# Optimization experiments

Measured on AMD Instinct MI355X. Metric: run time of the kernel, lower is better.

Reference implementation:

```python
import jax, jax.numpy as jnp
import numpy as np

CAPACITY_FACTOR = 1.25


def setup_inputs() -> dict:
    key = jax.random.key(0)
    k1, k2, k3, k4 = jax.random.split(key, 4)
    B, T, H = 2, 2048, 1024
    E, F = 8, 2048
    x = jax.random.normal(k1, (B, T, H), dtype=jnp.float32)
    Wr = jax.random.normal(k2, (H, E), dtype=jnp.float32) * 0.02
    W1 = jax.random.normal(k3, (E, H, 2 * F), dtype=jnp.float32) * 0.02
    W2 = jax.random.normal(k4, (E, F, H), dtype=jnp.float32) * 0.02
    return {"x": x, "Wr": Wr, "W1": W1, "W2": W2}


def _moe_forward(x, Wr, W1, W2):
    B, T, H = x.shape
    E = Wr.shape[1]
    N = B * T
    cap = max(1, int(CAPACITY_FACTOR * (N * 2 / E)))  # static (shape-derived)

    flat_x = x.reshape(N, H)
    logits = flat_x @ Wr                      # [N, E] (train=False: no noise)
    gate = jax.nn.softmax(logits, axis=-1)
    top2_val, top2_idx = jax.lax.top_k(gate, 2)   # [N,2]

    # --- capacity bookkeeping, matching the torch sequential fill order ---
    e0, e1 = top2_idx[:, 0], top2_idx[:, 1]
    oh0 = jax.nn.one_hot(e0, E, dtype=jnp.int32)  # [N,E]
    oh1 = jax.nn.one_hot(e1, E, dtype=jnp.int32)
    # rank of each token within its expert's k=0 queue (flattened token order)
    pos0 = jnp.take_along_axis(jnp.cumsum(oh0, axis=0), top2_idx[:, :1], axis=1)[:, 0] - 1
    count0 = oh0.sum(axis=0)                      # tokens routed top-1 per expert
    used0 = jnp.minimum(count0, cap)              # slots consumed in k=0 pass
    keep0 = pos0 < cap
    # k=1 pass starts after the slots used by k=0
    pos1 = jnp.take_along_axis(jnp.cumsum(oh1, axis=0), top2_idx[:, 1:2], axis=1)[:, 0] - 1
    pos1 = pos1 + used0[e1]
    keep1 = pos1 < cap

    dummy = E * cap  # drop slot
    slot0 = jnp.where(keep0, e0 * cap + pos0, dummy)
    slot1 = jnp.where(keep1, e1 * cap + pos1, dummy)

    # --- dispatch: [E*cap+1, H] buffer (last row is the drop slot) ---
    buf = jnp.zeros((E * cap + 1, H), dtype=x.dtype)
    buf = buf.at[slot0].set(flat_x).at[slot1].set(flat_x)
    xe = buf[: E * cap].reshape(E, cap, H)

    # --- grouped expert FFN (SwiGLU) ---
    h = jnp.einsum("ech,ehf->ecf", xe, W1)        # [E, cap, 2F]
    a, b = jnp.split(h, 2, axis=-1)
    act = jax.nn.silu(a) * b                      # [E, cap, F]
    out = jnp.einsum("ecf,efh->ech", act, W2)     # [E, cap, H]
    out_flat = out.reshape(E * cap, H)

    # --- combine: gather back per token, weighted by gate values ---
    g0 = out_flat[jnp.where(keep0, slot0, 0)] * keep0[:, None]
    g1 = out_flat[jnp.where(keep1, slot1, 0)] * keep1[:, None]
    y = g0 * top2_val[:, 0:1] + g1 * top2_val[:, 1:2]
    y = y.reshape(B, T, H)

    # --- balance loss ---
    me = 1e-9
    prob_per_expert = gate.mean(axis=0)                 # == mean over (B,T)
    used1 = (oh1 * keep1[:, None].astype(jnp.int32)).sum(axis=0)
    used = (used0 + used1).astype(gate.dtype)
    frac_used = jnp.maximum(used, me) / (N * 2 + me)
    balance_loss = (prob_per_expert * frac_used).sum() * E
    return y, balance_loss


def reference(x, Wr, W1, W2):
    return _moe_forward(x, Wr, W1, W2)
```

## Files before the change

### kernel.cpp

```cpp
#include <hip/hip_runtime.h>
#include <cstdint>

#define E_    8
#define H_    1024
#define F_    2048
#define NTOK  4096
#define CAP   1280
#define ECAP  (E_*CAP)

typedef unsigned short u16;
typedef __attribute__((ext_vector_type(8))) short bf16x8;
typedef __attribute__((ext_vector_type(4))) float f32x4;
typedef __attribute__((ext_vector_type(4))) unsigned short u16x4;

__device__ __forceinline__ u16 f2bf(float f) {
  union { float f; uint32_t u; } v; v.f = f;
  uint32_t r = v.u + 0x7fffu + ((v.u >> 16) & 1u);
  return (u16)(r >> 16);
}

__device__ __forceinline__ void gld16(const void* gsrc, void* ldst) {
  auto g = reinterpret_cast<const __attribute__((address_space(1))) uint32_t*>(
      reinterpret_cast<uintptr_t>(gsrc));
  auto l = reinterpret_cast<__attribute__((address_space(3))) uint32_t*>(
      reinterpret_cast<uintptr_t>(ldst));
  __builtin_amdgcn_global_load_lds(g, l, 16, 0, 0);
}

__device__ __forceinline__ int swz(int row, int chunk) {
  return row * 64 + ((chunk ^ (row & 7)) * 8);
}

__global__ __launch_bounds__(256) void prep_kernel(const float* __restrict__ W1,
                                                   const float* __restrict__ W2,
                                                   u16* __restrict__ W1T,
                                                   u16* __restrict__ W2T,
                                                   const float* __restrict__ x,
                                                   const float* __restrict__ Wr,
                                                   int* __restrict__ e0o, int* __restrict__ e1o,
                                                   float* __restrict__ v0o, float* __restrict__ v1o,
                                                   float* __restrict__ partial) {
  int b = blockIdx.x;
  if (b < 12288) {
    __shared__ float tile[64][65];
    const float* in; u16* outp; int R, C, rt, ct;
    if (b < 8192) {
      int slab = b >> 10, t = b & 1023;
      rt = t >> 6; ct = t & 63;
      R = H_; C = 2 * F_;
      in = W1 + (size_t)slab * R * C;
      outp = W1T + (size_t)slab * R * C;
    } else {
      int bb = b - 8192;
      int slab = bb >> 9, t = bb & 511;
      rt = t >> 4; ct = t & 15;
      R = F_; C = H_;
      in = W2 + (size_t)slab * R * C;
      outp = W2T + (size_t)slab * R * C;
    }
    int r0 = rt * 64, c0 = ct * 64;
    int tx = threadIdx.x & 15, ty = threadIdx.x >> 4;
#pragma unroll
    for (int i = 0; i < 4; i++) {
      int row = ty + 16 * i;
      float4 v = *(const float4*)(in + (size_t)(r0 + row) * C + c0 + tx * 4);
      tile[row][tx * 4 + 0] = v.x;
      tile[row][tx * 4 + 1] = v.y;
      tile[row][tx * 4 + 2] = v.z;
      tile[row][tx * 4 + 3] = v.w;
    }
    __syncthreads();
#pragma unroll
    for (int i = 0; i < 4; i++) {
      int c = ty + 16 * i;
      u16x4 bq;
      bq.x = f2bf(tile[tx * 4 + 0][c]);
      bq.y = f2bf(tile[tx * 4 + 1][c]);
      bq.z = f2bf(tile[tx * 4 + 2][c]);
      bq.w = f2bf(tile[tx * 4 + 3][c]);
      *(u16x4*)(outp + (size_t)(c0 + c) * R + r0 + tx * 4) = bq;
    }
  } else {
    int blk = b - 12288;
    int w = threadIdx.x >> 6, l = threadIdx.x & 63;
    int t = blk * 4 + w;
    const float* xr = x + (size_t)t * H_;
    float acc[8] = {0.f,0.f,0.f,0.f,0.f,0.f,0.f,0.f};
#pragma unroll
    for (int it = 0; it < 16; ++it) {
      int h = it * 64 + l;
      float xv = xr[h];
      const float4* wr = (const float4*)(Wr + h * 8);
      float4 wa = wr[0], wb = wr[1];
      acc[0] += xv * wa.x; acc[1] += xv * wa.y; acc[2] += xv * wa.z; acc[3] += xv * wa.w;
      acc[4] += xv * wb.x; acc[5] += xv * wb.y; acc[6] += xv * wb.z; acc[7] += xv * wb.w;
    }
#pragma unroll
    for (int e = 0; e < 8; ++e)
#pragma unroll
      for (int off = 32; off; off >>= 1)
        acc[e] += __shfl_xor(acc[e], off);

    __shared__ float pg[4][8];
    if (l == 0) {
      float mx = acc[0];
#pragma unroll
      for (int e = 1; e < 8; ++e) mx = fmaxf(mx, acc[e]);
      float g[8], s = 0.f;
#pragma unroll
      for (int e = 0; e < 8; ++e) { g[e] = __expf(acc[e] - mx); s += g[e]; }
      float inv = 1.f / s;
#pragma unroll
      for (int e = 0; e < 8; ++e) g[e] *= inv;
      int b0 = 0; float m0 = g[0];
#pragma unroll
      for (int e = 1; e < 8; ++e) if (g[e] > m0) { m0 = g[e]; b0 = e; }
      int b1 = -1; float m1 = -1.f;
#pragma unroll
      for (int e = 0; e < 8; ++e) if (e != b0 && g[e] > m1) { m1 = g[e]; b1 = e; }
      e0o[t] = b0; e1o[t] = b1; v0o[t] = m0; v1o[t] = m1;
#pragma unroll
      for (int e = 0; e < 8; ++e) pg[w][e] = g[e];
    }
    __syncthreads();
    if (threadIdx.x < 8) {
      int e = threadIdx.x;
      partial[blk * 8 + e] = pg[0][e] + pg[1][e] + pg[2][e] + pg[3][e];
    }
  }
}

__global__ __launch_bounds__(256) void scan_kernel(const int* __restrict__ e0i, const int* __restrict__ e1i,
                                                   const float* __restrict__ partial,
                                                   int* __restrict__ slot0, int* __restrict__ slot1,
                                                   int* __restrict__ used_out,
                                                   float* __restrict__ bl_out) {
  __shared__ int c0[256][8], c1[256][8];
  __shared__ float gs[256][8];
  __shared__ int used0_s[8], tot1_s[8];
  int tid = threadIdx.x;

  int le0[16], le1[16];
  int lc0[8] = {0,0,0,0,0,0,0,0}, lc1[8] = {0,0,0,0,0,0,0,0};
  for (int i = 0; i < 16; ++i) {
    int t = tid * 16 + i;
    le0[i] = e0i[t]; le1[i] = e1i[t];
    lc0[le0[i]]++; lc1[le1[i]]++;
  }
#pragma unroll
  for (int e = 0; e < 8; ++e) { c0[tid][e] = lc0[e]; c1[tid][e] = lc1[e]; }

  float g[8] = {0.f,0.f,0.f,0.f,0.f,0.f,0.f,0.f};
  for (int rr = 0; rr < 4; ++rr)
#pragma unroll
    for (int e = 0; e < 8; ++e) g[e] += partial[(tid + rr * 256) * 8 + e];
#pragma unroll
  for (int e = 0; e < 8; ++e) gs[tid][e] = g[e];
  __syncthreads();

  for (int d = 1; d < 256; d <<= 1) {
    int t0[8], t1[8];
    bool a = (tid >= d);
    if (a) {
#pragma unroll
      for (int e = 0; e < 8; ++e) { t0[e] = c0[tid - d][e]; t1[e] = c1[tid - d][e]; }
    }
    __syncthreads();
    if (a) {
#pragma unroll
      for (int e = 0; e < 8; ++e) { c0[tid][e] += t0[e]; c1[tid][e] += t1[e]; }
    }
    __syncthreads();
  }
  for (int s = 128; s > 0; s >>= 1) {
    if (tid < s)
#pragma unroll
      for (int e = 0; e < 8; ++e) gs[tid][e] += gs[tid + s][e];
    __syncthreads();
  }
  if (tid < 8) {
    int e = tid;
    int u0 = min(c0[255][e], CAP);
    int t1 = c1[255][e];
    used0_s[e] = u0;
    tot1_s[e] = t1;
    used_out[e] = u0 + min(t1, max(0, CAP - u0));
  }
  __syncthreads();

  int ex0[8], ex1[8];
#pragma unroll
  for (int e = 0; e < 8; ++e) { ex0[e] = c0[tid][e] - lc0[e]; ex1[e] = c1[tid][e] - lc1[e]; }
  int r0c[8] = {0,0,0,0,0,0,0,0}, r1c[8] = {0,0,0,0,0,0,0,0};
  for (int i = 0; i < 16; ++i) {
    int t = tid * 16 + i;
    int e = le0[i];
    int pos = ex0[e] + r0c[e]; r0c[e]++;
    slot0[t] = (pos < CAP) ? (e * CAP + pos) : -1;
    e = le1[i];
    pos = ex1[e] + r1c[e] + used0_s[e]; r1c[e]++;
    slot1[t] = (pos < CAP) ? (e * CAP + pos) : -1;
  }

  if (tid == 0) {
    float bl = 0.f;
    for (int e = 0; e < 8; ++e) {
      int u1 = min(tot1_s[e], max(0, CAP - used0_s[e]));
      float used = (float)(used0_s[e] + u1);
      float fu = fmaxf(used, 1e-9f) / (8192.f + 1e-9f);
      bl += (gs[0][e] / (float)NTOK) * fu;
    }
    bl_out[0] = bl * 8.f;
  }
}

__global__ __launch_bounds__(256) void scatter_kernel(const float* __restrict__ x,
                                                      const int* __restrict__ slot0,
                                                      const int* __restrict__ slot1,
                                                      u16* __restrict__ xe) {
  int t = blockIdx.x, tid = threadIdx.x;
  float4 vv = *(const float4*)(x + (size_t)t * H_ + tid * 4);
  u16x4 b;
  b.x = f2bf(vv.x); b.y = f2bf(vv.y); b.z = f2bf(vv.z); b.w = f2bf(vv.w);
  int s0 = slot0[t], s1 = slot1[t];
  if (s0 >= 0) *(u16x4*)(xe + (size_t)s0 * H_ + tid * 4) = b;
  if (s1 >= 0) *(u16x4*)(xe + (size_t)s1 * H_ + tid * 4) = b;
}

__global__ __launch_bounds__(256, 2) void gemm1_kernel(const u16* __restrict__ xe,
                                                       const u16* __restrict__ W1T,
                                                       const int* __restrict__ used_tot,
                                                       u16* __restrict__ act) {
  const int mbase = blockIdx.y * 128;
  const int e = mbase / 1280;
  if (mbase - e * 1280 >= used_tot[e]) return;

  __shared__ u16 As[128 * 64];
  __shared__ u16 Bsa[64 * 64];
  __shared__ u16 Bsb[64 * 64];
  const int tid = threadIdx.x;
  const int w = tid >> 6, l = tid & 63;
  const int wm = w & 1, wn = w >> 1;
  const int nbase = blockIdx.x * 64;
  const u16* Ap = xe + (size_t)mbase * H_;
  const u16* Ba = W1T + (size_t)e * 4096 * H_ + (size_t)nbase * H_;
  const u16* Bb = Ba + (size_t)F_ * H_;
  const int lrow = l >> 3;
  const int lcol = (((l & 7) ^ lrow) * 8);

  f32x4 acca[4][2] = {};
  f32x4 accb[4][2] = {};

  for (int kt = 0; kt < 16; ++kt) {
    int k0 = kt * 64;
#pragma unroll
    for (int r = 0; r < 4; ++r) {
      int row0 = w * 32 + r * 8;
      gld16(Ap + (size_t)(row0 + lrow) * H_ + k0 + lcol, &As[row0 * 64]);
    }
#pragma unroll
    for (int r = 0; r < 2; ++r) {
      int row0 = w * 16 + r * 8;
      gld16(Ba + (size_t)(row0 + lrow) * H_ + k0 + lcol, &Bsa[row0 * 64]);
      gld16(Bb + (size_t)(row0 + lrow) * H_ + k0 + lcol, &Bsb[row0 * 64]);
    }
    __syncthreads();
#pragma unroll
    for (int kk = 0; kk < 64; kk += 32) {
      const int ck = (kk >> 3) + (l >> 4);
      bf16x8 af[4], ba[2], bb[2];
#pragma unroll
      for (int i = 0; i < 4; ++i)
        af[i] = *(const bf16x8*)&As[swz(wm * 64 + i * 16 + (l & 15), ck)];
#pragma unroll
      for (int j = 0; j < 2; ++j) {
        ba[j] = *(const bf16x8*)&Bsa[swz(wn * 32 + j * 16 + (l & 15), ck)];
        bb[j] = *(const bf16x8*)&Bsb[swz(wn * 32 + j * 16 + (l & 15), ck)];
      }
#pragma unroll
      for (int i = 0; i < 4; ++i)
#pragma unroll
        for (int j = 0; j < 2; ++j) {
          acca[i][j] = __builtin_amdgcn_mfma_f32_16x16x32_bf16(af[i], ba[j], acca[i][j], 0, 0, 0);
          accb[i][j] = __builtin_amdgcn_mfma_f32_16x16x32_bf16(af[i], bb[j], accb[i][j], 0, 0, 0);
        }
    }
    __syncthreads();
  }
#pragma unroll
  for (int i = 0; i < 4; ++i)
#pragma unroll
    for (int j = 0; j < 2; ++j)
#pragma unroll
      for (int r = 0; r < 4; ++r) {
        int m = mbase + wm * 64 + i * 16 + (l >> 4) * 4 + r;
        int f = nbase + wn * 32 + j * 16 + (l & 15);
        float a = acca[i][j][r];
        float b = accb[i][j][r];
        float s = a / (1.f + __expf(-a));
        act[(size_t)m * F_ + f] = f2bf(s * b);
      }
}

__global__ __launch_bounds__(256, 2) void gemm2_kernel(const u16* __restrict__ act,
                                                       const u16* __restrict__ W2T,
                                                       const int* __restrict__ used_tot,
                                                       float* __restrict__ outb) {
  const int mbase = blockIdx.y * 128;
  const int e = mbase / 1280;
  if (mbase - e * 1280 >= used_tot[e]) return;

  __shared__ u16 As[128 * 64];
  __shared__ u16 Bs[128 * 64];
  const int tid = threadIdx.x;
  const int w = tid >> 6, l = tid & 63;
  const int wm = w & 1, wn = w >> 1;
  const int nbase = blockIdx.x * 128;
  const u16* Ap = act + (size_t)mbase * F_;
  const u16* Bp = W2T + (size_t)e * H_ * F_ + (size_t)nbase * F_;
  const int lrow = l >> 3;
  const int lcol = (((l & 7) ^ lrow) * 8);

  f32x4 acc[4][4] = {};

  for (int kt = 0; kt < 32; ++kt) {
    int k0 = kt * 64;
#pragma unroll
    for (int r = 0; r < 4; ++r) {
      int row0 = w * 32 + r * 8;
      gld16(Ap + (size_t)(row0 + lrow) * F_ + k0 + lcol, &As[row0 * 64]);
      gld16(Bp + (size_t)(row0 + lrow) * F_ + k0 + lcol, &Bs[row0 * 64]);
    }
    __syncthreads();
#pragma unroll
    for (int kk = 0; kk < 64; kk += 32) {
      const int ck = (kk >> 3) + (l >> 4);
      bf16x8 af[4], bf[4];
#pragma unroll
      for (int i = 0; i < 4; ++i)
        af[i] = *(const bf16x8*)&As[swz(wm * 64 + i * 16 + (l & 15), ck)];
#pragma unroll
      for (int j = 0; j < 4; ++j)
        bf[j] = *(const bf16x8*)&Bs[swz(wn * 64 + j * 16 + (l & 15), ck)];
#pragma unroll
      for (int i = 0; i < 4; ++i)
#pragma unroll
        for (int j = 0; j < 4; ++j)
          acc[i][j] = __builtin_amdgcn_mfma_f32_16x16x32_bf16(af[i], bf[j], acc[i][j], 0, 0, 0);
    }
    __syncthreads();
  }
#pragma unroll
  for (int i = 0; i < 4; ++i)
#pragma unroll
    for (int j = 0; j < 4; ++j)
#pragma unroll
      for (int r = 0; r < 4; ++r) {
        int m = mbase + wm * 64 + i * 16 + (l >> 4) * 4 + r;
        int n = nbase + wn * 64 + j * 16 + (l & 15);
        outb[(size_t)m * H_ + n] = acc[i][j][r];
      }
}

__global__ __launch_bounds__(256) void combine_kernel(const float* __restrict__ outb,
                                                      const int* __restrict__ slot0,
                                                      const int* __restrict__ slot1,
                                                      const float* __restrict__ v0,
                                                      const float* __restrict__ v1,
                                                      float* __restrict__ y) {
  int t = blockIdx.x, tid = threadIdx.x;
  int s0 = slot0[t], s1 = slot1[t];
  float w0 = v0[t], w1 = v1[t];
  float4 r; r.x = 0.f; r.y = 0.f; r.z = 0.f; r.w = 0.f;
  if (s0 >= 0) {
    float4 a = *(const float4*)(outb + (size_t)s0 * H_ + tid * 4);
    r.x += w0 * a.x; r.y += w0 * a.y; r.z += w0 * a.z; r.w += w0 * a.w;
  }
  if (s1 >= 0) {
    float4 a = *(const float4*)(outb + (size_t)s1 * H_ + tid * 4);
    r.x += w1 * a.x; r.y += w1 * a.y; r.z += w1 * a.z; r.w += w1 * a.w;
  }
  *(float4*)(y + (size_t)t * H_ + tid * 4) = r;
}

#define OFF_W1T   ((size_t)0)
#define OFF_W2T   ((size_t)67108864)
#define OFF_XE    ((size_t)100663296)
#define OFF_ACT   ((size_t)121634816)
#define OFF_OUTB  ((size_t)163577856)
#define OFF_SLOT0 ((size_t)205520896)
#define OFF_SLOT1 ((size_t)205537280)
#define OFF_V0    ((size_t)205553664)
#define OFF_V1    ((size_t)205570048)
#define OFF_E0    ((size_t)205586432)
#define OFF_E1    ((size_t)205602816)
#define OFF_PART  ((size_t)205619200)
#define OFF_USED  ((size_t)205651968)

extern "C" void kernel_launch(void* const* d_in, const int* in_sizes, int n_in,
                              void* d_out, int out_size, void* d_ws, size_t ws_size,
                              hipStream_t stream) {
  const float* x  = (const float*)d_in[0];
  const float* Wr = (const float*)d_in[1];
  const float* W1 = (const float*)d_in[2];
  const float* W2 = (const float*)d_in[3];
  float* out = (float*)d_out;

  uint8_t* ws = (uint8_t*)d_ws;
  u16*   W1T   = (u16*)(ws + OFF_W1T);
  u16*   W2T   = (u16*)(ws + OFF_W2T);
  u16*   xe    = (u16*)(ws + OFF_XE);
  u16*   act   = (u16*)(ws + OFF_ACT);
  float* outb  = (float*)(ws + OFF_OUTB);
  int*   slot0 = (int*)(ws + OFF_SLOT0);
  int*   slot1 = (int*)(ws + OFF_SLOT1);
  float* v0    = (float*)(ws + OFF_V0);
  float* v1    = (float*)(ws + OFF_V1);
  int*   e0    = (int*)(ws + OFF_E0);
  int*   e1    = (int*)(ws + OFF_E1);
  float* part  = (float*)(ws + OFF_PART);
  int*   used  = (int*)(ws + OFF_USED);

  prep_kernel<<<13312, 256, 0, stream>>>(W1, W2, W1T, W2T, x, Wr, e0, e1, v0, v1, part);

  scan_kernel<<<1, 256, 0, stream>>>(e0, e1, part, slot0, slot1, used, out + (size_t)NTOK * H_);
  scatter_kernel<<<NTOK, 256, 0, stream>>>(x, slot0, slot1, xe);

  gemm1_kernel<<<dim3(F_ / 64, ECAP / 128), 256, 0, stream>>>(xe, W1T, used, act);
  gemm2_kernel<<<dim3(H_ / 128, ECAP / 128), 256, 0, stream>>>(act, W2T, used, outb);

  combine_kernel<<<NTOK, 256, 0, stream>>>(outb, slot0, slot1, v0, v1, out);
}
```

Before: 221.8 us.

## Overlap W2 transpose-convert with first expert GEMM in a merged kernel

Moves the W2 fp32-to-bf16 transpose out of the prep kernel and into the first expert GEMM launch, interleaving 5 GEMM blocks with 8 transpose blocks per group of 13. The aim is to hide the memory-bound W2 conversion behind the compute-bound GEMM1 and shorten the prep kernel on the critical path before scan/scatter. The cost is that LDS is now 32KB for every block and the old minimum-occupancy launch bound is dropped. GEMM and transpose blocks also contend for bandwidth.

```diff
diff --git a/kernel.cpp b/kernel.cpp
--- a/kernel.cpp
+++ b/kernel.cpp
@@ -32,32 +32,20 @@
 }
 
 __global__ __launch_bounds__(256) void prep_kernel(const float* __restrict__ W1,
-                                                   const float* __restrict__ W2,
                                                    u16* __restrict__ W1T,
-                                                   u16* __restrict__ W2T,
                                                    const float* __restrict__ x,
                                                    const float* __restrict__ Wr,
                                                    int* __restrict__ e0o, int* __restrict__ e1o,
                                                    float* __restrict__ v0o, float* __restrict__ v1o,
                                                    float* __restrict__ partial) {
   int b = blockIdx.x;
-  if (b < 12288) {
+  if (b < 8192) {
     __shared__ float tile[64][65];
-    const float* in; u16* outp; int R, C, rt, ct;
-    if (b < 8192) {
-      int slab = b >> 10, t = b & 1023;
-      rt = t >> 6; ct = t & 63;
-      R = H_; C = 2 * F_;
-      in = W1 + (size_t)slab * R * C;
-      outp = W1T + (size_t)slab * R * C;
-    } else {
-      int bb = b - 8192;
-      int slab = bb >> 9, t = bb & 511;
-      rt = t >> 4; ct = t & 15;
-      R = F_; C = H_;
-      in = W2 + (size_t)slab * R * C;
-      outp = W2T + (size_t)slab * R * C;
-    }
+    int slab = b >> 10, t = b & 1023;
+    int rt = t >> 6, ct = t & 63;
+    const int R = H_, C = 2 * F_;
+    const float* in = W1 + (size_t)slab * R * C;
+    u16* outp = W1T + (size_t)slab * R * C;
     int r0 = rt * 64, c0 = ct * 64;
     int tx = threadIdx.x & 15, ty = threadIdx.x >> 4;
 #pragma unroll
@@ -81,7 +69,7 @@
       *(u16x4*)(outp + (size_t)(c0 + c) * R + r0 + tx * 4) = bq;
     }
   } else {
-    int blk = b - 12288;
+    int blk = b - 8192;
     int w = threadIdx.x >> 6, l = threadIdx.x & 63;
     int t = blk * 4 + w;
     const float* xr = x + (size_t)t * H_;
@@ -227,79 +215,119 @@
   if (s1 >= 0) *(u16x4*)(xe + (size_t)s1 * H_ + tid * 4) = b;
 }
 
-__global__ __launch_bounds__(256, 2) void gemm1_kernel(const u16* __restrict__ xe,
-                                                       const u16* __restrict__ W1T,
-                                                       const int* __restrict__ used_tot,
-                                                       u16* __restrict__ act) {
-  const int mbase = blockIdx.y * 128;
-  const int e = mbase / 1280;
-  if (mbase - e * 1280 >= used_tot[e]) return;
-
-  __shared__ u16 As[128 * 64];
-  __shared__ u16 Bsa[64 * 64];
-  __shared__ u16 Bsb[64 * 64];
-  const int tid = threadIdx.x;
-  const int w = tid >> 6, l = tid & 63;
-  const int wm = w & 1, wn = w >> 1;
-  const int nbase = blockIdx.x * 64;
-  const u16* Ap = xe + (size_t)mbase * H_;
-  const u16* Ba = W1T + (size_t)e * 4096 * H_ + (size_t)nbase * H_;
-  const u16* Bb = Ba + (size_t)F_ * H_;
-  const int lrow = l >> 3;
-  const int lcol = (((l & 7) ^ lrow) * 8);
-
-  f32x4 acca[4][2] = {};
-  f32x4 accb[4][2] = {};
-
-  for (int kt = 0; kt < 16; ++kt) {
-    int k0 = kt * 64;
-#pragma unroll
-    for (int r = 0; r < 4; ++r) {
-      int row0 = w * 32 + r * 8;
-      gld16(Ap + (size_t)(row0 + lrow) * H_ + k0 + lcol, &As[row0 * 64]);
-    }
-#pragma unroll
-    for (int r = 0; r < 2; ++r) {
-      int row0 = w * 16 + r * 8;
-      gld16(Ba + (size_t)(row0 + lrow) * H_ + k0 + lcol, &Bsa[row0 * 64]);
-      gld16(Bb + (size_t)(row0 + lrow) * H_ + k0 + lcol, &Bsb[row0 * 64]);
-    }
-    __syncthreads();
-#pragma unroll
-    for (int kk = 0; kk < 64; kk += 32) {
-      const int ck = (kk >> 3) + (l >> 4);
-      bf16x8 af[4], ba[2], bb[2];
-#pragma unroll
-      for (int i = 0; i < 4; ++i)
-        af[i] = *(const bf16x8*)&As[swz(wm * 64 + i * 16 + (l & 15), ck)];
-#pragma unroll
-      for (int j = 0; j < 2; ++j) {
-        ba[j] = *(const bf16x8*)&Bsa[swz(wn * 32 + j * 16 + (l & 15), ck)];
-        bb[j] = *(const bf16x8*)&Bsb[swz(wn * 32 + j * 16 + (l & 15), ck)];
+__global__ __launch_bounds__(256) void ffn1_kernel(const u16* __restrict__ xe,
+                                                   const u16* __restrict__ W1T,
+                                                   const int* __restrict__ used_tot,
+                                                   u16* __restrict__ act,
+                                                   const float* __restrict__ W2,
+                                                   u16* __restrict__ W2T) {
+  __shared__ char lds[32768];
+  const int g = blockIdx.x / 13, r = blockIdx.x % 13;
+
+  if (r < 5) {
+    const int id = g * 5 + r;
+    const int bx = id & 31;
+    const int by = id >> 5;
+    const int mbase = by * 128;
+    const int e = mbase / 1280;
+    if (mbase - e * 1280 >= used_tot[e]) return;
+
+    u16* As  = (u16*)lds;
+    u16* Bsa = (u16*)(lds + 16384);
+    u16* Bsb = (u16*)(lds + 24576);
+    const int tid = threadIdx.x;
+    const int w = tid >> 6, l = tid & 63;
+    const int wm = w & 1, wn = w >> 1;
+    const int nbase = bx * 64;
+    const u16* Ap = xe + (size_t)mbase * H_;
+    const u16* Ba = W1T + (size_t)e * 4096 * H_ + (size_t)nbase * H_;
+    const u16* Bb = Ba + (size_t)F_ * H_;
+    const int lrow = l >> 3;
+    const int lcol = (((l & 7) ^ lrow) * 8);
+
+    f32x4 acca[4][2] = {};
+    f32x4 accb[4][2] = {};
+
+    for (int kt = 0; kt < 16; ++kt) {
+      int k0 = kt * 64;
+#pragma unroll
+      for (int rr = 0; rr < 4; ++rr) {
+        int row0 = w * 32 + rr * 8;
+        gld16(Ap + (size_t)(row0 + lrow) * H_ + k0 + lcol, &As[row0 * 64]);
       }
 #pragma unroll
-      for (int i = 0; i < 4; ++i)
+      for (int rr = 0; rr < 2; ++rr) {
+        int row0 = w * 16 + rr * 8;
+        gld16(Ba + (size_t)(row0 + lrow) * H_ + k0 + lcol, &Bsa[row0 * 64]);
+        gld16(Bb + (size_t)(row0 + lrow) * H_ + k0 + lcol, &Bsb[row0 * 64]);
+      }
+      __syncthreads();
+#pragma unroll
+      for (int kk = 0; kk < 64; kk += 32) {
+        const int ck = (kk >> 3) + (l >> 4);
+        bf16x8 af[4], ba[2], bb[2];
+#pragma unroll
+        for (int i = 0; i < 4; ++i)
+          af[i] = *(const bf16x8*)&As[swz(wm * 64 + i * 16 + (l & 15), ck)];
 #pragma unroll
         for (int j = 0; j < 2; ++j) {
-          acca[i][j] = __builtin_amdgcn_mfma_f32_16x16x32_bf16(af[i], ba[j], acca[i][j], 0, 0, 0);
-          accb[i][j] = __builtin_amdgcn_mfma_f32_16x16x32_bf16(af[i], bb[j], accb[i][j], 0, 0, 0);
+          ba[j] = *(const bf16x8*)&Bsa[swz(wn * 32 + j * 16 + (l & 15), ck)];
+          bb[j] = *(const bf16x8*)&Bsb[swz(wn * 32 + j * 16 + (l & 15), ck)];
         }
-    }
-    __syncthreads();
-  }
-#pragma unroll
-  for (int i = 0; i < 4; ++i)
-#pragma unroll
-    for (int j = 0; j < 2; ++j)
-#pragma unroll
-      for (int r = 0; r < 4; ++r) {
-        int m = mbase + wm * 64 + i * 16 + (l >> 4) * 4 + r;
-        int f = nbase + wn * 32 + j * 16 + (l & 15);
-        float a = acca[i][j][r];
-        float b = accb[i][j][r];
-        float s = a / (1.f + __expf(-a));
-        act[(size_t)m * F_ + f] = f2bf(s * b);
+#pragma unroll
+        for (int i = 0; i < 4; ++i)
+#pragma unroll
+          for (int j = 0; j < 2; ++j) {
+            acca[i][j] = __builtin_amdgcn_mfma_f32_16x16x32_bf16(af[i], ba[j], acca[i][j], 0, 0, 0);
+            accb[i][j] = __builtin_amdgcn_mfma_f32_16x16x32_bf16(af[i], bb[j], accb[i][j], 0, 0, 0);
+          }
       }
+      __syncthreads();
+    }
+#pragma unroll
+    for (int i = 0; i < 4; ++i)
+#pragma unroll
+      for (int j = 0; j < 2; ++j)
+#pragma unroll
+        for (int rr = 0; rr < 4; ++rr) {
+          int m = mbase + wm * 64 + i * 16 + (l >> 4) * 4 + rr;
+          int f = nbase + wn * 32 + j * 16 + (l & 15);
+          float a = acca[i][j][rr];
+          float b = accb[i][j][rr];
+          float s = a / (1.f + __expf(-a));
+          act[(size_t)m * F_ + f] = f2bf(s * b);
+        }
+  } else {
+    const int id = g * 8 + (r - 5);
+    float (*tile)[65] = reinterpret_cast<float(*)[65]>(lds);
+    int slab = id >> 9, t = id & 511;
+    int rt = t >> 4, ct = t & 15;
+    const int R = F_, C = H_;
+    const float* in = W2 + (size_t)slab * R * C;
+    u16* outp = W2T + (size_t)slab * R * C;
+    int r0 = rt * 64, c0 = ct * 64;
+    int tx = threadIdx.x & 15, ty = threadIdx.x >> 4;
+#pragma unroll
+    for (int i = 0; i < 4; i++) {
+      int row = ty + 16 * i;
+      float4 v = *(const float4*)(in + (size_t)(r0 + row) * C + c0 + tx * 4);
+      tile[row][tx * 4 + 0] = v.x;
+      tile[row][tx * 4 + 1] = v.y;
+      tile[row][tx * 4 + 2] = v.z;
+      tile[row][tx * 4 + 3] = v.w;
+    }
+    __syncthreads();
+#pragma unroll
+    for (int i = 0; i < 4; i++) {
+      int c = ty + 16 * i;
+      u16x4 bq;
+      bq.x = f2bf(tile[tx * 4 + 0][c]);
+      bq.y = f2bf(tile[tx * 4 + 1][c]);
+      bq.z = f2bf(tile[tx * 4 + 2][c]);
+      bq.w = f2bf(tile[tx * 4 + 3][c]);
+      *(u16x4*)(outp + (size_t)(c0 + c) * R + r0 + tx * 4) = bq;
+    }
+  }
 }
 
 __global__ __launch_bounds__(256, 2) void gemm2_kernel(const u16* __restrict__ act,
@@ -421,12 +449,13 @@
   float* part  = (float*)(ws + OFF_PART);
   int*   used  = (int*)(ws + OFF_USED);
 
-  prep_kernel<<<13312, 256, 0, stream>>>(W1, W2, W1T, W2T, x, Wr, e0, e1, v0, v1, part);
+  prep_kernel<<<9216, 256, 0, stream>>>(W1, W1T, x, Wr, e0, e1, v0, v1, part);
 
   scan_kernel<<<1, 256, 0, stream>>>(e0, e1, part, slot0, slot1, used, out + (size_t)NTOK * H_);
   scatter_kernel<<<NTOK, 256, 0, stream>>>(x, slot0, slot1, xe);
 
-  gemm1_kernel<<<dim3(F_ / 64, ECAP / 128), 256, 0, stream>>>(xe, W1T, used, act);
+  ffn1_kernel<<<6656, 256, 0, stream>>>(xe, W1T, used, act, W2, W2T);
+
   gemm2_kernel<<<dim3(H_ / 128, ECAP / 128), 256, 0, stream>>>(act, W2T, used, outb);
 
   combine_kernel<<<NTOK, 256, 0, stream>>>(outb, slot0, slot1, v0, v1, out);
```

Measured after the change: 225.8 us. No clear change (+1.8%).
